# Optimization experiments

Measured on AMD Instinct MI355X. Metric: run time of the kernel, lower is better.

## Reference

```python
import jax, jax.numpy as jnp
import numpy as np

V = 32000   # vocab
D = 1024    # dim
H = 16      # query heads
HKV = 8     # kv heads (GQA)
DH = D // H # head dim = 64
L = 2       # layers
FF = 3584   # expert hidden dim
E = 8       # experts
K = 2       # top-k
EPS = 1e-5
BASE = 1000000.0
B, S = 1, 2048


def setup_inputs() -> dict:
    key = jax.random.key(0)
    ks = jax.random.split(key, 10)
    s = 0.02
    return {
        "x": jax.random.randint(ks[0], (B, S), 0, V, dtype=jnp.int64) if jax.config.jax_enable_x64 else jax.random.randint(ks[0], (B, S), 0, V),
        "emb": jax.random.normal(ks[1], (V, D), jnp.float32) * s,
        "ln_w": jnp.ones((L, D), jnp.float32),
        "ffln_w": jnp.ones((L, D), jnp.float32),
        "wq": jax.random.normal(ks[2], (L, D, H * DH), jnp.float32) * s,
        "wk": jax.random.normal(ks[3], (L, D, HKV * DH), jnp.float32) * s,
        "wv": jax.random.normal(ks[4], (L, D, HKV * DH), jnp.float32) * s,
        "wo": jax.random.normal(ks[5], (L, H * DH, D), jnp.float32) * s,
        "gate_w": jax.random.normal(ks[6], (L, E, D), jnp.float32) * s,
        "w1": jax.random.normal(ks[7], (L, E, FF, D), jnp.float32) * s,
        "w2": jax.random.normal(ks[8], (L, E, D, FF), jnp.float32) * s,
        "w3": jax.random.normal(ks[9], (L, E, FF, D), jnp.float32) * s,
        "dec_norm_w": jnp.ones((D,), jnp.float32),
    }


def rmsnorm(x, w):
    # LayerNormParameterized(use_mean=False, shift=False) == RMSNorm, pow in fp32
    xf = x.astype(jnp.float32)
    var = jnp.mean(xf * xf, axis=-1, keepdims=True)
    return ((xf * jax.lax.rsqrt(var + EPS)).astype(x.dtype)) * w


def rope(xh, pos):
    # interleaved (complex-pair) rotary embedding, xh: [B, S, h, DH]
    half = DH // 2
    freqs = 1.0 / (BASE ** (jnp.arange(0, half, dtype=jnp.float32) * 2.0 / DH))
    ang = pos[:, None] * freqs[None, :]                       # [S, half]
    cos = jnp.cos(ang)[None, :, None, :]
    sin = jnp.sin(ang)[None, :, None, :]
    x1 = xh[..., 0::2]
    x2 = xh[..., 1::2]
    out = jnp.stack([x1 * cos - x2 * sin, x1 * sin + x2 * cos], axis=-1)
    return out.reshape(xh.shape)


def reference(x, emb, ln_w, ffln_w, wq, wk, wv, wo, gate_w, w1, w2, w3, dec_norm_w):
    h = emb[x]                                                # [B, S, D]
    pos = jnp.arange(S, dtype=jnp.float32)
    causal = jnp.tril(jnp.ones((S, S), bool))[None, None]     # [1,1,S,S]
    scale = 1.0 / np.sqrt(DH).astype(np.float32)
    for i in range(L):
        # --- attention sub-layer ---
        res = h
        xn = rmsnorm(h, ln_w[i])
        q = rope((xn @ wq[i]).reshape(B, S, H, DH), pos)
        k = rope((xn @ wk[i]).reshape(B, S, HKV, DH), pos)
        v = (xn @ wv[i]).reshape(B, S, HKV, DH)
        rep = H // HKV
        k = jnp.repeat(k, rep, axis=2)                        # [B,S,H,DH]
        v = jnp.repeat(v, rep, axis=2)
        scores = jnp.einsum('bqhd,bkhd->bhqk', q, k) * scale
        scores = jnp.where(causal, scores, jnp.float32(-1e9))
        att = jax.nn.softmax(scores, axis=-1)
        o = jnp.einsum('bhqk,bkhd->bqhd', att, v).reshape(B, S, H * DH) @ wo[i]
        h = res + o
        # --- MoE FFN sub-layer ---
        res = h
        xn = rmsnorm(h, ffln_w[i]).reshape(B * S, D)          # [T, D]
        logits = xn @ gate_w[i].T                             # [T, E]
        gates = jax.nn.softmax(logits, axis=-1)
        topw, topi = jax.lax.top_k(gates, K)                  # [T, K]
        topw = topw / jnp.sum(topw, axis=-1, keepdims=True)
        # dense combine weights [T, E] (zero for unselected experts)
        cw = jnp.einsum('tk,tke->te', topw, jax.nn.one_hot(topi, E, dtype=topw.dtype))
        y = jnp.zeros_like(xn)
        for e in range(E):                                    # fixed small expert loop
            ye = (jax.nn.silu(xn @ w1[i, e].T) * (xn @ w3[i, e].T)) @ w2[i, e].T
            y = y + cw[:, e:e + 1] * ye
        h = res + y.reshape(B, S, D)
    return rmsnorm(h, dec_norm_w)
```

## Files before the change

### kernel.cpp

```cpp
#include <hip/hip_runtime.h>

using u16 = unsigned short;
using u32 = unsigned int;

#define TT 2048
#define DM 1024
#define NH 16
#define NKV 8
#define DHD 64
#define FFD 3584
#define NE 8

typedef __bf16 bf16x8 __attribute__((ext_vector_type(8)));
typedef float f32x4 __attribute__((ext_vector_type(4)));

__device__ __forceinline__ u16 f2bf(float x){
  return __builtin_bit_cast(u16, (__bf16)x);
}
__device__ __forceinline__ float bf2f(u16 h){
  return (float)__builtin_bit_cast(__bf16, h);
}
__device__ __forceinline__ f32x4 mfma16(bf16x8 a, bf16x8 b, f32x4 c){
  return __builtin_amdgcn_mfma_f32_16x16x32_bf16(a, b, c, 0, 0, 0);
}
__device__ __forceinline__ uint4 packhi8v(float4 a, float4 b){
  u16 h0=f2bf(a.x),h1=f2bf(a.y),h2=f2bf(a.z),h3=f2bf(a.w);
  u16 h4=f2bf(b.x),h5=f2bf(b.y),h6=f2bf(b.z),h7=f2bf(b.w);
  return make_uint4((u32)h0|((u32)h1<<16),(u32)h2|((u32)h3<<16),
                    (u32)h4|((u32)h5<<16),(u32)h6|((u32)h7<<16));
}
__device__ __forceinline__ uint4 packlo8v(float4 a, float4 b){
  u16 l0=f2bf(a.x-bf2f(f2bf(a.x))),l1=f2bf(a.y-bf2f(f2bf(a.y)));
  u16 l2=f2bf(a.z-bf2f(f2bf(a.z))),l3=f2bf(a.w-bf2f(f2bf(a.w)));
  u16 l4=f2bf(b.x-bf2f(f2bf(b.x))),l5=f2bf(b.y-bf2f(f2bf(b.y)));
  u16 l6=f2bf(b.z-bf2f(f2bf(b.z))),l7=f2bf(b.w-bf2f(f2bf(b.w)));
  return make_uint4((u32)l0|((u32)l1<<16),(u32)l2|((u32)l3<<16),
                    (u32)l4|((u32)l5<<16),(u32)l6|((u32)l7<<16));
}

#define SWZR(r) ((((r)>>1) ^ ((r)>>3)) & 3)
#define SWC(r,c) ((((c) ^ SWZR(r))) * 8)

__device__ __forceinline__ void glds16(const u16* g, u16* l){
  __builtin_amdgcn_global_load_lds(
      (const __attribute__((address_space(1))) void*)g,
      (__attribute__((address_space(3))) void*)l,
      16, 0, 0);
}

__global__ __launch_bounds__(256) void k_embed(const int* __restrict__ x,
    const float* __restrict__ emb, float* __restrict__ h){
  int t = blockIdx.x;
  int d = threadIdx.x * 4;
  float4 v = *reinterpret_cast<const float4*>(emb + (size_t)x[t] * DM + d);
  *reinterpret_cast<float4*>(h + (size_t)t * DM + d) = v;
}

template<int OUTF32>
__global__ __launch_bounds__(256) void k_rmsnorm(const float* __restrict__ in,
    const float* __restrict__ w, u16* __restrict__ oh, u16* __restrict__ ol,
    float* __restrict__ of){
  int t = blockIdx.x;
  int d4 = threadIdx.x * 4;
  float4 xv = *reinterpret_cast<const float4*>(in + (size_t)t * DM + d4);
  float ss = xv.x*xv.x + xv.y*xv.y + xv.z*xv.z + xv.w*xv.w;
#pragma unroll
  for (int m = 1; m < 64; m <<= 1) ss += __shfl_xor(ss, m);
  __shared__ float sred[4];
  if ((threadIdx.x & 63) == 0) sred[threadIdx.x >> 6] = ss;
  __syncthreads();
  float tot = sred[0] + sred[1] + sred[2] + sred[3];
  float r = 1.0f / sqrtf(tot * (1.0f / DM) + 1e-5f);
  float vv[4] = {xv.x, xv.y, xv.z, xv.w};
#pragma unroll
  for (int jj = 0; jj < 4; jj++){
    float xn = (vv[jj] * r) * w[d4 + jj];
    size_t a = (size_t)t * DM + d4 + jj;
    if constexpr (OUTF32){
      of[a] = xn;
    } else {
      u16 hi = f2bf(xn);
      oh[a] = hi;
      ol[a] = f2bf(xn - bf2f(hi));
    }
  }
}

__global__ __launch_bounds__(256) void k_trig(float* __restrict__ ct, float* __restrict__ st){
  int idx = blockIdx.x * 256 + threadIdx.x;
  int j = idx & 31;
  int s = idx >> 5;
  float xe = (float)j * 0.03125f;
  float yf = (float)pow(1.0e6, (double)xe);
  float fr = 1.0f / yf;
  float ang = (float)s * fr;
  double ad = (double)ang;
  ct[idx] = (float)cos(ad);
  st[idx] = (float)sin(ad);
}

template<int NHD>
__global__ __launch_bounds__(256) void k_rope(const float* __restrict__ in,
    const float* __restrict__ ct, const float* __restrict__ st,
    u16* __restrict__ oh, u16* __restrict__ ol){
  int idx = blockIdx.x * 256 + threadIdx.x;
  int j = idx & 31;
  int hd = (idx >> 5) % NHD;
  int s = idx / (32 * NHD);
  size_t base = ((size_t)s * NHD + hd) * 64 + 2 * j;
  float x1 = in[base], x2 = in[base + 1];
  int ti = (s << 5) | j;
  float c  = ct[ti];
  float sn = st[ti];
  float o1 = x1 * c - x2 * sn;
  float o2 = x1 * sn + x2 * c;
  u16 h1 = f2bf(o1), h2 = f2bf(o2);
  oh[base]     = h1; ol[base]     = f2bf(o1 - bf2f(h1));
  oh[base + 1] = h2; ol[base + 1] = f2bf(o2 - bf2f(h2));
}

__global__ __launch_bounds__(256) void k_splitbuf(const float* __restrict__ in,
    u16* __restrict__ oh, u16* __restrict__ ol, int n){
  int i = blockIdx.x * 256 + threadIdx.x;
  if (i < n){
    float x = in[i];
    u16 hi = f2bf(x);
    oh[i] = hi;
    ol[i] = f2bf(x - bf2f(hi));
  }
}

__global__ __launch_bounds__(256) void k_gate(const u16* __restrict__ xh,
    const u16* __restrict__ xl, const float* __restrict__ gw,
    int* __restrict__ topi, float* __restrict__ topw, int* __restrict__ cnt){
  int wv = threadIdx.x >> 6, lane = threadIdx.x & 63;
  int t = blockIdx.x * 4 + wv;
  float x[16];
#pragma unroll
  for (int i = 0; i < 16; i++){
    size_t a = (size_t)t * DM + lane + 64 * i;
    x[i] = bf2f(xh[a]) + bf2f(xl[a]);
  }
  float lgt[8];
#pragma unroll
  for (int e = 0; e < 8; e++){
    float s = 0.f;
#pragma unroll
    for (int i = 0; i < 16; i++) s += x[i] * gw[(size_t)e * DM + lane + 64 * i];
#pragma unroll
    for (int m = 1; m < 64; m <<= 1) s += __shfl_xor(s, m);
    lgt[e] = s;
  }
  float mx = lgt[0];
#pragma unroll
  for (int e = 1; e < 8; e++) mx = fmaxf(mx, lgt[e]);
  float p[8]; float sum = 0.f;
#pragma unroll
  for (int e = 0; e < 8; e++){ p[e] = expf(lgt[e] - mx); sum += p[e]; }
  float g[8];
#pragma unroll
  for (int e = 0; e < 8; e++) g[e] = p[e] / sum;
  int t0 = 0; float b0 = g[0];
#pragma unroll
  for (int e = 1; e < 8; e++) if (g[e] > b0){ b0 = g[e]; t0 = e; }
  int t1 = -1; float b1 = -1.f;
#pragma unroll
  for (int e = 0; e < 8; e++) if (e != t0 && g[e] > b1){ b1 = g[e]; t1 = e; }
  float ssum = b0 + b1;
  float w0 = b0 / ssum, w1 = b1 / ssum;
  if (lane == 0 && t < TT){
    topi[2*t] = t0; topi[2*t+1] = t1;
    topw[2*t] = w0; topw[2*t+1] = w1;
    atomicAdd(&cnt[t0], 1);
    atomicAdd(&cnt[t1], 1);
  }
}

__global__ void k_zero8(int* cnt){ if (threadIdx.x < 8) cnt[threadIdx.x] = 0; }

__global__ void k_scan(const int* __restrict__ cnt, int* __restrict__ offp, int* __restrict__ cur){
  if (threadIdx.x == 0){
    int r = 0;
    for (int e = 0; e < 8; e++){ offp[e] = r; r += cnt[e]; }
  }
  if (threadIdx.x < 8) cur[threadIdx.x] = 0;
}

__global__ __launch_bounds__(256) void k_scatter(const int* __restrict__ topi,
    const float* __restrict__ topw, const int* __restrict__ offp, int* __restrict__ cur,
    int* __restrict__ ftok, float* __restrict__ fwt){
  int t = blockIdx.x * 256 + threadIdx.x;
  if (t < TT){
#pragma unroll
    for (int j = 0; j < 2; j++){
      int e = topi[2*t + j];
      int p = atomicAdd(&cur[e], 1);
      ftok[offp[e] + p] = t;
      fwt[offp[e] + p] = topw[2*t + j];
    }
  }
}

#define GLDSA(BUF, KK) do { \
    glds16(Ah + gaA0 + (KK), (u16*)&Ash[BUF][awr0][0]); \
    glds16(Ah + gaA1 + (KK), (u16*)&Ash[BUF][awr1][0]); \
    if constexpr (SPLIT){ \
      glds16(Al + gaA0 + (KK), (u16*)&Asl[BUF][awr0][0]); \
      glds16(Al + gaA1 + (KK), (u16*)&Asl[BUF][awr1][0]); \
    } \
  } while(0)

#define GPRELOADB(KK) do { \
    if constexpr (BLAYOUT == 0){ \
      const float* bp_ = Bw + (size_t)(n0 + br0) * K + (KK) + cb8; \
      pB0 = *reinterpret_cast<const float4*>(bp_); \
      pB1 = *reinterpret_cast<const float4*>(bp_ + 4); \
      if constexpr (TN == 128){ \
        const float* bp2_ = Bw + (size_t)(n0 + br1) * K + (KK) + cb8; \
        pB2 = *reinterpret_cast<const float4*>(bp2_); \
        pB3 = *reinterpret_cast<const float4*>(bp2_ + 4); \
      } \
      if constexpr (DUAL){ \
        const float* bq_ = B3w + (size_t)(n0 + br0) * K + (KK) + cb8; \
        pB2 = *reinterpret_cast<const float4*>(bq_); \
        pB3 = *reinterpret_cast<const float4*>(bq_ + 4); \
      } \
    } else { \
      pB0 = *reinterpret_cast<const float4*>(Bw + (size_t)((KK) + kk1) * Nq + n0 + nn1); \
      pB1 = *reinterpret_cast<const float4*>(Bw + (size_t)((KK) + 16 + kk1) * Nq + n0 + nn1); \
    } \
  } while(0)

#define GSTOREB() do { \
    if constexpr (BLAYOUT == 0){ \
      *reinterpret_cast<uint4*>(&Bh1[br0][swB0]) = packhi8v(pB0, pB1); \
      if constexpr (SPLIT) *reinterpret_cast<uint4*>(&Bl1[br0][swB0]) = packlo8v(pB0, pB1); \
      if constexpr (TN == 128){ \
        *reinterpret_cast<uint4*>(&Bh1[br1][swB1]) = packhi8v(pB2, pB3); \
        if constexpr (SPLIT) *reinterpret_cast<uint4*>(&Bl1[br1][swB1]) = packlo8v(pB2, pB3); \
      } \
      if constexpr (DUAL){ \
        *reinterpret_cast<uint4*>(&Bh3[br0][swB0]) = packhi8v(pB2, pB3); \
        if constexpr (SPLIT) *reinterpret_cast<uint4*>(&Bl3[br0][swB0]) = packlo8v(pB2, pB3); \
      } \
    } else { \
      const float* q0 = reinterpret_cast<const float*>(&pB0); \
      const float* q1 = reinterpret_cast<const float*>(&pB1); \
      const int ch0 = kk1 >> 3, off0 = kk1 & 7; \
      _Pragma("unroll") \
      for (int j = 0; j < 4; j++){ \
        int row = nn1 + j; \
        int c0 = SWC(row, ch0) + off0; \
        int c1 = SWC(row, ch0 + 2) + off0; \
        u16 h0 = f2bf(q0[j]); \
        Bh1[row][c0] = h0; \
        if constexpr (SPLIT) Bl1[row][c0] = f2bf(q0[j] - bf2f(h0)); \
        u16 h1 = f2bf(q1[j]); \
        Bh1[row][c1] = h1; \
        if constexpr (SPLIT) Bl1[row][c1] = f2bf(q1[j] - bf2f(h1)); \
      } \
    } \
  } while(0)

#define MFMA_PHASE(CURB) do { \
    bf16x8 af[4], afl[4]; \
    _Pragma("unroll") \
    for (int m = 0; m < 4; m++){ \
      int Ra = wr*64 + m*16 + lr; \
      int sa = SWC(Ra, lg); \
      af[m] = *reinterpret_cast<const bf16x8*>(&Ash[CURB][Ra][sa]); \
      if constexpr (SPLIT) \
        afl[m] = *reinterpret_cast<const bf16x8*>(&Asl[CURB][Ra][sa]); \
    } \
    _Pragma("unroll") \
    for (int n = 0; n < NF; n++){ \
      int Rb = wc*(TN/2) + n*16 + lr; \
      int sb = SWC(Rb, lg); \
      bf16x8 b1 = *reinterpret_cast<const bf16x8*>(&Bh1[Rb][sb]); \
      _Pragma("unroll") \
      for (int m = 0; m < 4; m++) acc[m][n] = mfma16(af[m], b1, acc[m][n]); \
      if constexpr (SPLIT){ \
        bf16x8 bl = *reinterpret_cast<const bf16x8*>(&Bl1[Rb][sb]); \
        _Pragma("unroll") \
        for (int m = 0; m < 4; m++){ \
          acc[m][n] = mfma16(af[m], bl, acc[m][n]); \
          acc[m][n] = mfma16(afl[m], b1, acc[m][n]); \
        } \
      } \
      if constexpr (DUAL){ \
        bf16x8 b3 = *reinterpret_cast<const bf16x8*>(&Bh3[Rb][sb]); \
        _Pragma("unroll") \
        for (int m = 0; m < 4; m++) acc3[m][n] = mfma16(af[m], b3, acc3[m][n]); \
        if constexpr (SPLIT){ \
          bf16x8 b3l = *reinterpret_cast<const bf16x8*>(&Bl3[Rb][sb]); \
          _Pragma("unroll") \
          for (int m = 0; m < 4; m++){ \
            acc3[m][n] = mfma16(af[m], b3l, acc3[m][n]); \
            acc3[m][n] = mfma16(afl[m], b3, acc3[m][n]); \
          } \
        } \
      } \
    } \
  } while(0)

template<int BLAYOUT, int EPI, int SPLIT, int DUAL, int TN, int KS>
__global__ __launch_bounds__(256) void k_gemm(
    const u16* __restrict__ Ah, const u16* __restrict__ Al,
    const float* __restrict__ Bw, const float* __restrict__ B3w,
    const float* __restrict__ Bw2, const float* __restrict__ Bw3,
    size_t strideB, int N, int K,
    float* __restrict__ Cf, int ldc,
    float* __restrict__ Cf2, float* __restrict__ Cf3,
    u16* __restrict__ Ch, u16* __restrict__ Cl,
    const int* __restrict__ cntp, const int* __restrict__ offp,
    const int* __restrict__ ftok, const float* __restrict__ fwt)
{
  static_assert(!(DUAL && TN != 64), "DUAL uses TN=64");
  static_assert(!(BLAYOUT == 1 && TN != 64), "BLAYOUT=1 uses TN=64");
  int cnt = TT, off = 0, ks = 0;
  if constexpr (EPI == 2 || EPI == 3){
    int e = blockIdx.z / KS;
    ks = blockIdx.z % KS;
    cnt = cntp[e]; off = offp[e];
    if ((int)blockIdx.y * 128 >= cnt) return;
    Bw += (size_t)e * strideB;
    if constexpr (DUAL) B3w += (size_t)e * strideB;
  } else if constexpr (KS > 1){
    ks = blockIdx.z;
  }
  __shared__ u16 Ash[2][128][32];
  __shared__ u16 Asl[SPLIT ? 2 : 1][SPLIT ? 128 : 1][32];
  __shared__ u16 Bh1[TN][32];
  __shared__ u16 Bl1[SPLIT ? TN : 1][32];
  __shared__ u16 Bh3[DUAL ? TN : 1][32];
  __shared__ u16 Bl3[(DUAL && SPLIT) ? TN : 1][32];

  const int tid = threadIdx.x;
  const int m0 = blockIdx.y * 128;

  int n0, Nq = N, ldq = ldc;
  float* Cq = Cf;
  if constexpr (EPI == 4){
    int bx = blockIdx.x;
    if (bx < 16){       n0 = bx * 64;        Nq = 1024; ldq = 1024; Cq = Cf;  }
    else if (bx < 24){  n0 = (bx - 16) * 64; Nq = 512;  ldq = 512;  Cq = Cf2; Bw = Bw2; }
    else {              n0 = (bx - 24) * 64; Nq = 512;  ldq = 512;  Cq = Cf3; Bw = Bw3; }
  } else {
    n0 = blockIdx.x * TN;
  }

  const int wid = tid >> 6, lane = tid & 63;
  const int wr = wid >> 1, wc = wid & 1;
  const int lr = lane & 15, lg = lane >> 4;
  constexpr int NF = TN / 32;

  const int awr0 = wid * 32;
  const int awr1 = wid * 32 + 16;
  const int rA0 = awr0 + (lane >> 2);
  const int rA1 = awr1 + (lane >> 2);
  const int cA0 = (lane & 3) ^ SWZR(rA0);
  const int cA1 = (lane & 3) ^ SWZR(rA1);
  int grA0, grA1;
  {
    int g0 = m0 + rA0, g1 = m0 + rA1;
    if constexpr (EPI == 2){
      grA0 = ftok[off + (g0 < cnt ? g0 : cnt - 1)];
      grA1 = ftok[off + (g1 < cnt ? g1 : cnt - 1)];
    } else if constexpr (EPI == 3){
      grA0 = off + (g0 < cnt ? g0 : cnt - 1);
      grA1 = off + (g1 < cnt ? g1 : cnt - 1);
    } else {
      grA0 = g0; grA1 = g1;
    }
  }
  const size_t gaA0 = (size_t)grA0 * K + cA0 * 8;
  const size_t gaA1 = (size_t)grA1 * K + cA1 * 8;

  const int br0 = tid >> 2;
  const int br1 = br0 + 64;
  const int cb8 = (tid & 3) * 8;
  const int swB0 = SWC(br0, tid & 3), swB1 = SWC(br1, tid & 3);
  const int kk1 = tid >> 4;
  const int nn1 = (tid & 15) * 4;

  f32x4 acc[4][NF];
  f32x4 acc3[DUAL ? 4 : 1][NF];
#pragma unroll
  for (int m = 0; m < 4; m++)
#pragma unroll
    for (int n = 0; n < NF; n++){
      acc[m][n] = f32x4{0.f,0.f,0.f,0.f};
      if constexpr (DUAL) acc3[m][n] = f32x4{0.f,0.f,0.f,0.f};
    }

  float4 pB0{}, pB1{}, pB2{}, pB3{};

  const int kbeg = ks * (K / KS);
  const int kend = kbeg + (K / KS);

  GLDSA(0, kbeg);
  GPRELOADB(kbeg);
  int cur = 0;
  for (int k0 = kbeg; k0 < kend; k0 += 32){
    GSTOREB();
    asm volatile("s_waitcnt vmcnt(0) lgkmcnt(0)" ::: "memory");
    __builtin_amdgcn_s_barrier();
    if (k0 + 32 < kend){
      GLDSA(cur ^ 1, k0 + 32);
      GPRELOADB(k0 + 32);
    }
    MFMA_PHASE(cur);
    __builtin_amdgcn_s_barrier();
    cur ^= 1;
  }

#pragma unroll
  for (int m = 0; m < 4; m++)
#pragma unroll
    for (int n = 0; n < NF; n++)
#pragma unroll
      for (int r = 0; r < 4; r++){
        int row = m0 + wr*64 + m*16 + lg*4 + r;
        int col = n0 + wc*(TN/2) + n*16 + lr;
        float v = acc[m][n][r];
        if constexpr (EPI == 0){
          Cf[(size_t)row * ldc + col] = v;
        } else if constexpr (EPI == 1){
          if constexpr (KS > 1) atomicAdd(&Cf[(size_t)row * ldc + col], v);
          else                  Cf[(size_t)row * ldc + col] += v;
        } else if constexpr (EPI == 2){
          if (row < cnt){
            float a3 = acc3[m][n][r];
            float s = v / (1.0f + expf(-v));
            float y = s * a3;
            u16 hi = f2bf(y);
            size_t oa = (size_t)(off + row) * ldc + col;
            Ch[oa] = hi;
            Cl[oa] = f2bf(y - bf2f(hi));
          }
        } else if constexpr (EPI == 3){
          if (row < cnt){
            int tok = ftok[off + row];
            float wgt = fwt[off + row];
            atomicAdd(&Cf[(size_t)tok * ldc + col], wgt * v);
          }
        } else {
          if constexpr (KS > 1) atomicAdd(&Cq[(size_t)row * ldq + col], v);
          else                  Cq[(size_t)row * ldq + col] = v;
        }
      }
}

__global__ __launch_bounds__(256) void k_attn(
    const u16* __restrict__ qh, const u16* __restrict__ ql,
    const u16* __restrict__ kh, const u16* __restrict__ kl,
    const u16* __restrict__ vh, const u16* __restrict__ vl,
    u16* __restrict__ aoh, u16* __restrict__ aol)
{
  const int h  = blockIdx.y;
  const int q0 = blockIdx.x * 64;
  const int hk = h >> 1;
  const int tid = threadIdx.x;
  const int wv = tid >> 6, lane = tid & 63;
  const int lr = lane & 15, lg = lane >> 4;
  const int qw0 = q0 + wv * 16;

  __shared__ u16 Khs[32][72], Kls[32][72];
  __shared__ u16 Vhs[64][40], Vls[64][40];
  __shared__ u16 Phs[4][16][40], Pls[4][16][40];

  bf16x8 qfh[2], qfl[2];
#pragma unroll
  for (int dc = 0; dc < 2; dc++){
    size_t qa = ((size_t)(qw0 + lr) * NH + h) * 64 + dc*32 + lg*8;
    qfh[dc] = *reinterpret_cast<const bf16x8*>(qh + qa);
    qfl[dc] = *reinterpret_cast<const bf16x8*>(ql + qa);
  }
  f32x4 oacc[4];
  float mrun[4], lrun[4];
#pragma unroll
  for (int r = 0; r < 4; r++){ mrun[r] = -1e30f; lrun[r] = 0.f; }
#pragma unroll
  for (int g = 0; g < 4; g++) oacc[g] = f32x4{0.f,0.f,0.f,0.f};

  const int nt = q0 / 32 + 2;
  for (int kt = 0; kt < nt; kt++){
    int kg = kt * 32;
    {
      int kk = tid >> 3, c8 = (tid & 7) * 8;
      size_t ka = ((size_t)(kg + kk) * NKV + hk) * 64 + c8;
      *reinterpret_cast<uint4*>(&Khs[kk][c8]) = *reinterpret_cast<const uint4*>(kh + ka);
      *reinterpret_cast<uint4*>(&Kls[kk][c8]) = *reinterpret_cast<const uint4*>(kl + ka);
      uint4 v1 = *reinterpret_cast<const uint4*>(vh + ka);
      uint4 v2 = *reinterpret_cast<const uint4*>(vl + ka);
      const u16* p1 = reinterpret_cast<const u16*>(&v1);
      const u16* p2 = reinterpret_cast<const u16*>(&v2);
#pragma unroll
      for (int j = 0; j < 8; j++){ Vhs[c8 + j][kk] = p1[j]; Vls[c8 + j][kk] = p2[j]; }
    }
    __syncthreads();

    f32x4 sc[2];
    sc[0] = f32x4{0.f,0.f,0.f,0.f};
    sc[1] = f32x4{0.f,0.f,0.f,0.f};
#pragma unroll
    for (int c = 0; c < 2; c++){
#pragma unroll
      for (int dc = 0; dc < 2; dc++){
        bf16x8 bh = *reinterpret_cast<const bf16x8*>(&Khs[c*16 + lr][dc*32 + lg*8]);
        bf16x8 bl = *reinterpret_cast<const bf16x8*>(&Kls[c*16 + lr][dc*32 + lg*8]);
        sc[c] = mfma16(qfh[dc], bh, sc[c]);
        sc[c] = mfma16(qfh[dc], bl, sc[c]);
        sc[c] = mfma16(qfl[dc], bh, sc[c]);
      }
    }
    float pnew[2][4], corr[4];
#pragma unroll
    for (int r = 0; r < 4; r++){
      int row = qw0 + lg*4 + r;
      float s0 = (kg + lr      <= row) ? sc[0][r] * 0.125f : -1e30f;
      float s1 = (kg + 16 + lr <= row) ? sc[1][r] * 0.125f : -1e30f;
      float tm = fmaxf(s0, s1);
#pragma unroll
      for (int m = 1; m < 16; m <<= 1) tm = fmaxf(tm, __shfl_xor(tm, m));
      float mnew = fmaxf(mrun[r], tm);
      corr[r] = expf(mrun[r] - mnew);
      float p0 = expf(s0 - mnew);
      float p1 = expf(s1 - mnew);
      pnew[0][r] = p0; pnew[1][r] = p1;
      float sm = p0 + p1;
#pragma unroll
      for (int m = 1; m < 16; m <<= 1) sm += __shfl_xor(sm, m);
      lrun[r] = lrun[r] * corr[r] + sm;
      mrun[r] = mnew;
    }
#pragma unroll
    for (int g = 0; g < 4; g++){
      f32x4 t = oacc[g];
#pragma unroll
      for (int r = 0; r < 4; r++) t[r] *= corr[r];
      oacc[g] = t;
    }
#pragma unroll
    for (int c = 0; c < 2; c++)
#pragma unroll
      for (int r = 0; r < 4; r++){
        float p = pnew[c][r];
        u16 hi = f2bf(p);
        Phs[wv][lg*4 + r][c*16 + lr] = hi;
        Pls[wv][lg*4 + r][c*16 + lr] = f2bf(p - bf2f(hi));
      }
    asm volatile("s_waitcnt lgkmcnt(0)" ::: "memory");
    __builtin_amdgcn_sched_barrier(0);
    bf16x8 pah = *reinterpret_cast<const bf16x8*>(&Phs[wv][lr][lg*8]);
    bf16x8 pal = *reinterpret_cast<const bf16x8*>(&Pls[wv][lr][lg*8]);
#pragma unroll
    for (int g = 0; g < 4; g++){
      bf16x8 vb1 = *reinterpret_cast<const bf16x8*>(&Vhs[g*16 + lr][lg*8]);
      bf16x8 vb2 = *reinterpret_cast<const bf16x8*>(&Vls[g*16 + lr][lg*8]);
      oacc[g] = mfma16(pah, vb1, oacc[g]);
      oacc[g] = mfma16(pah, vb2, oacc[g]);
      oacc[g] = mfma16(pal, vb1, oacc[g]);
    }
    __syncthreads();
  }
#pragma unroll
  for (int g = 0; g < 4; g++)
#pragma unroll
    for (int r = 0; r < 4; r++){
      int row = qw0 + lg*4 + r;
      float v = oacc[g][r] / lrun[r];
      u16 hi = f2bf(v);
      size_t oa = ((size_t)row * NH + h) * 64 + g*16 + lr;
      aoh[oa] = hi;
      aol[oa] = f2bf(v - bf2f(hi));
    }
}

extern "C" void kernel_launch(void* const* d_in, const int* in_sizes, int n_in,
                              void* d_out, int out_size, void* d_ws, size_t ws_size,
                              hipStream_t stream){
  const int*   x     = (const int*)d_in[0];
  const float* emb   = (const float*)d_in[1];
  const float* lnw   = (const float*)d_in[2];
  const float* fflnw = (const float*)d_in[3];
  const float* wq    = (const float*)d_in[4];
  const float* wk    = (const float*)d_in[5];
  const float* wvp   = (const float*)d_in[6];
  const float* wo    = (const float*)d_in[7];
  const float* gw    = (const float*)d_in[8];
  const float* w1    = (const float*)d_in[9];
  const float* w2    = (const float*)d_in[10];
  const float* w3    = (const float*)d_in[11];
  const float* dnw   = (const float*)d_in[12];
  float* out = (float*)d_out;

  char* p = (char*)d_ws;
  auto alloc = [&](size_t bytes)->char*{
    char* r = p; p += (bytes + 255) & ~(size_t)255; return r;
  };
  float* h    = (float*)alloc((size_t)TT * DM * 4);
  float* qbuf = (float*)alloc((size_t)TT * 1024 * 4);
  float* kbuf = (float*)alloc((size_t)TT * 512 * 4);
  float* vbuf = (float*)alloc((size_t)TT * 512 * 4);
  u16* xnh = (u16*)alloc((size_t)TT * DM * 2);
  u16* xnl = (u16*)alloc((size_t)TT * DM * 2);
  u16* qhb = (u16*)alloc((size_t)TT * 1024 * 2);
  u16* qlb = (u16*)alloc((size_t)TT * 1024 * 2);
  u16* khb = (u16*)alloc((size_t)TT * 512 * 2);
  u16* klb = (u16*)alloc((size_t)TT * 512 * 2);
  u16* vhb = (u16*)alloc((size_t)TT * 512 * 2);
  u16* vlb = (u16*)alloc((size_t)TT * 512 * 2);
  u16* aoh = (u16*)alloc((size_t)TT * 1024 * 2);
  u16* aol = (u16*)alloc((size_t)TT * 1024 * 2);
  u16* acth = (u16*)alloc((size_t)2 * TT * FFD * 2);
  u16* actl = (u16*)alloc((size_t)2 * TT * FFD * 2);
  int*   topi = (int*)alloc((size_t)2 * TT * 4);
  float* topw = (float*)alloc((size_t)2 * TT * 4);
  int* cnt  = (int*)alloc(64);
  int* offe = (int*)alloc(64);
  int* cur  = (int*)alloc(64);
  int*   ftok = (int*)alloc((size_t)2 * TT * 4);
  float* fwt  = (float*)alloc((size_t)2 * TT * 4);
  float* ctab = (float*)aoh;
  float* stab = (float*)aol;

  k_embed<<<TT, 256, 0, stream>>>(x, emb, h);

  for (int i = 0; i < 2; i++){
    const float* wq_i = wq + (size_t)i * DM * 1024;
    const float* wk_i = wk + (size_t)i * DM * 512;
    const float* wv_i = wvp + (size_t)i * DM * 512;
    const float* wo_i = wo + (size_t)i * 1024 * DM;
    const float* w1_i = w1 + (size_t)i * NE * FFD * DM;
    const float* w2_i = w2 + (size_t)i * NE * DM * FFD;
    const float* w3_i = w3 + (size_t)i * NE * FFD * DM;

    k_rmsnorm<0><<<TT, 256, 0, stream>>>(h, lnw + i * DM, xnh, xnl, nullptr);

    hipMemsetAsync(qbuf, 0, (size_t)TT * 1024 * 4, stream);
    hipMemsetAsync(kbuf, 0, (size_t)TT * 512 * 4, stream);
    hipMemsetAsync(vbuf, 0, (size_t)TT * 512 * 4, stream);
    k_gemm<1,4,1,0,64,2><<<dim3(32,16,2), 256, 0, stream>>>(xnh, xnl,
        wq_i, nullptr, wk_i, wv_i, 0, 1024, DM,
        qbuf, 1024, kbuf, vbuf, nullptr, nullptr, nullptr, nullptr, nullptr, nullptr);

    k_trig<<<TT * 32 / 256, 256, 0, stream>>>(ctab, stab);
    k_rope<16><<<4096, 256, 0, stream>>>(qbuf, ctab, stab, qhb, qlb);
    k_rope<8><<<2048, 256, 0, stream>>>(kbuf, ctab, stab, khb, klb);
    k_splitbuf<<<4096, 256, 0, stream>>>(vbuf, vhb, vlb, TT * 512);

    k_attn<<<dim3(32,16,1), 256, 0, stream>>>(qhb, qlb, khb, klb, vhb, vlb, aoh, aol);

    k_gemm<1,1,1,0,64,2><<<dim3(16,16,2), 256, 0, stream>>>(aoh, aol,
        wo_i, nullptr, nullptr, nullptr, 0, DM, 1024,
        h, DM, nullptr, nullptr, nullptr, nullptr, nullptr, nullptr, nullptr, nullptr);

    k_rmsnorm<0><<<TT, 256, 0, stream>>>(h, fflnw + i * DM, xnh, xnl, nullptr);

    k_zero8<<<1, 64, 0, stream>>>(cnt);
    k_gate<<<TT/4, 256, 0, stream>>>(xnh, xnl, gw + (size_t)i * NE * DM, topi, topw, cnt);
    k_scan<<<1, 64, 0, stream>>>(cnt, offe, cur);
    k_scatter<<<8, 256, 0, stream>>>(topi, topw, offe, cur, ftok, fwt);

    if (i == 0){
      k_gemm<0,2,1,1,64,1><<<dim3(FFD/64,16,8), 256, 0, stream>>>(xnh, xnl,
          w1_i, w3_i, nullptr, nullptr, (size_t)FFD * DM, FFD, DM,
          nullptr, FFD, nullptr, nullptr, acth, actl, cnt, offe, ftok, fwt);
      k_gemm<0,3,1,0,128,4><<<dim3(DM/128,16,32), 256, 0, stream>>>(acth, actl,
          w2_i, nullptr, nullptr, nullptr, (size_t)DM * FFD, DM, FFD,
          h, DM, nullptr, nullptr, nullptr, nullptr, cnt, offe, ftok, fwt);
    } else {
      k_gemm<0,2,0,1,64,1><<<dim3(FFD/64,16,8), 256, 0, stream>>>(xnh, xnl,
          w1_i, w3_i, nullptr, nullptr, (size_t)FFD * DM, FFD, DM,
          nullptr, FFD, nullptr, nullptr, acth, actl, cnt, offe, ftok, fwt);
      k_gemm<0,3,0,0,128,4><<<dim3(DM/128,16,32), 256, 0, stream>>>(acth, actl,
          w2_i, nullptr, nullptr, nullptr, (size_t)DM * FFD, DM, FFD,
          h, DM, nullptr, nullptr, nullptr, nullptr, cnt, offe, ftok, fwt);
    }
  }

  k_rmsnorm<1><<<TT, 256, 0, stream>>>(h, dnw, nullptr, nullptr, out);
}
```

Measured before the change: 1.479 ms.

## Double-buffer B register prefetch to keep weight loads two K-steps ahead

The GEMM main loop now keeps two sets of B prefetch registers and unrolls by two K-steps. Global weight loads are issued two iterations ahead, and the wait uses a partial vmcnt so that the newest B loads can stay in flight across the barrier. The goal is to hide global-load latency on the fp32 weight stream. The cost is extra VGPRs for the second register set, which may lower occupancy. The correctness of the vmcnt counts depends on the order in which loads are issued.

Result: slower. 1.691 ms (+14.4%).

```diff
diff --git a/kernel.cpp b/kernel.cpp
--- a/kernel.cpp
+++ b/kernel.cpp
@@ -210,42 +210,42 @@
     } \
   } while(0)
 
-#define GPRELOADB(KK) do { \
+#define GPRELOADB(S, KK) do { \
     if constexpr (BLAYOUT == 0){ \
       const float* bp_ = Bw + (size_t)(n0 + br0) * K + (KK) + cb8; \
-      pB0 = *reinterpret_cast<const float4*>(bp_); \
-      pB1 = *reinterpret_cast<const float4*>(bp_ + 4); \
+      S##B0 = *reinterpret_cast<const float4*>(bp_); \
+      S##B1 = *reinterpret_cast<const float4*>(bp_ + 4); \
       if constexpr (TN == 128){ \
         const float* bp2_ = Bw + (size_t)(n0 + br1) * K + (KK) + cb8; \
-        pB2 = *reinterpret_cast<const float4*>(bp2_); \
-        pB3 = *reinterpret_cast<const float4*>(bp2_ + 4); \
+        S##B2 = *reinterpret_cast<const float4*>(bp2_); \
+        S##B3 = *reinterpret_cast<const float4*>(bp2_ + 4); \
       } \
       if constexpr (DUAL){ \
         const float* bq_ = B3w + (size_t)(n0 + br0) * K + (KK) + cb8; \
-        pB2 = *reinterpret_cast<const float4*>(bq_); \
-        pB3 = *reinterpret_cast<const float4*>(bq_ + 4); \
+        S##B2 = *reinterpret_cast<const float4*>(bq_); \
+        S##B3 = *reinterpret_cast<const float4*>(bq_ + 4); \
       } \
     } else { \
-      pB0 = *reinterpret_cast<const float4*>(Bw + (size_t)((KK) + kk1) * Nq + n0 + nn1); \
-      pB1 = *reinterpret_cast<const float4*>(Bw + (size_t)((KK) + 16 + kk1) * Nq + n0 + nn1); \
+      S##B0 = *reinterpret_cast<const float4*>(Bw + (size_t)((KK) + kk1) * Nq + n0 + nn1); \
+      S##B1 = *reinterpret_cast<const float4*>(Bw + (size_t)((KK) + 16 + kk1) * Nq + n0 + nn1); \
     } \
   } while(0)
 
-#define GSTOREB() do { \
+#define GSTOREB(S) do { \
     if constexpr (BLAYOUT == 0){ \
-      *reinterpret_cast<uint4*>(&Bh1[br0][swB0]) = packhi8v(pB0, pB1); \
-      if constexpr (SPLIT) *reinterpret_cast<uint4*>(&Bl1[br0][swB0]) = packlo8v(pB0, pB1); \
+      *reinterpret_cast<uint4*>(&Bh1[br0][swB0]) = packhi8v(S##B0, S##B1); \
+      if constexpr (SPLIT) *reinterpret_cast<uint4*>(&Bl1[br0][swB0]) = packlo8v(S##B0, S##B1); \
       if constexpr (TN == 128){ \
-        *reinterpret_cast<uint4*>(&Bh1[br1][swB1]) = packhi8v(pB2, pB3); \
-        if constexpr (SPLIT) *reinterpret_cast<uint4*>(&Bl1[br1][swB1]) = packlo8v(pB2, pB3); \
+        *reinterpret_cast<uint4*>(&Bh1[br1][swB1]) = packhi8v(S##B2, S##B3); \
+        if constexpr (SPLIT) *reinterpret_cast<uint4*>(&Bl1[br1][swB1]) = packlo8v(S##B2, S##B3); \
       } \
       if constexpr (DUAL){ \
-        *reinterpret_cast<uint4*>(&Bh3[br0][swB0]) = packhi8v(pB2, pB3); \
-        if constexpr (SPLIT) *reinterpret_cast<uint4*>(&Bl3[br0][swB0]) = packlo8v(pB2, pB3); \
+        *reinterpret_cast<uint4*>(&Bh3[br0][swB0]) = packhi8v(S##B2, S##B3); \
+        if constexpr (SPLIT) *reinterpret_cast<uint4*>(&Bl3[br0][swB0]) = packlo8v(S##B2, S##B3); \
       } \
     } else { \
-      const float* q0 = reinterpret_cast<const float*>(&pB0); \
-      const float* q1 = reinterpret_cast<const float*>(&pB1); \
+      const float* q0 = reinterpret_cast<const float*>(&S##B0); \
+      const float* q1 = reinterpret_cast<const float*>(&S##B1); \
       const int ch0 = kk1 >> 3, off0 = kk1 & 7; \
       _Pragma("unroll") \
       for (int j = 0; j < 4; j++){ \
@@ -261,6 +261,12 @@
       } \
     } \
   } while(0)
+
+#define WAITN() do { \
+    if constexpr (NBLD == 4) asm volatile("s_waitcnt vmcnt(4) lgkmcnt(0)" ::: "memory"); \
+    else                     asm volatile("s_waitcnt vmcnt(2) lgkmcnt(0)" ::: "memory"); \
+  } while(0)
+#define WAIT0() asm volatile("s_waitcnt vmcnt(0) lgkmcnt(0)" ::: "memory")
 
 #define MFMA_PHASE(CURB) do { \
     bf16x8 af[4], afl[4]; \
@@ -317,6 +323,7 @@
 {
   static_assert(!(DUAL && TN != 64), "DUAL uses TN=64");
   static_assert(!(BLAYOUT == 1 && TN != 64), "BLAYOUT=1 uses TN=64");
+  constexpr int NBLD = (BLAYOUT == 0 && (DUAL || TN == 128)) ? 4 : 2;
   int cnt = TT, off = 0, ks = 0;
   if constexpr (EPI == 2 || EPI == 3){
     int e = blockIdx.z / KS;
@@ -393,25 +400,39 @@
       if constexpr (DUAL) acc3[m][n] = f32x4{0.f,0.f,0.f,0.f};
     }
 
-  float4 pB0{}, pB1{}, pB2{}, pB3{};
+  float4 aB0{}, aB1{}, aB2{}, aB3{};
+  float4 bB0{}, bB1{}, bB2{}, bB3{};
 
   const int kbeg = ks * (K / KS);
   const int kend = kbeg + (K / KS);
 
   GLDSA(0, kbeg);
-  GPRELOADB(kbeg);
+  GPRELOADB(a, kbeg);
+  if (kbeg + 32 < kend) GPRELOADB(b, kbeg + 32);
   int cur = 0;
-  for (int k0 = kbeg; k0 < kend; k0 += 32){
-    GSTOREB();
-    asm volatile("s_waitcnt vmcnt(0) lgkmcnt(0)" ::: "memory");
-    __builtin_amdgcn_s_barrier();
+  for (int k0 = kbeg; k0 < kend; k0 += 64){
+    {
+      const bool pre = (k0 + 64 < kend);
+      GSTOREB(a);
+      if (pre) WAITN(); else WAIT0();
+      __builtin_amdgcn_s_barrier();
+      if (k0 + 32 < kend) GLDSA(cur ^ 1, k0 + 32);
+      if (pre) GPRELOADB(a, k0 + 64);
+      MFMA_PHASE(cur);
+      __builtin_amdgcn_s_barrier();
+      cur ^= 1;
+    }
     if (k0 + 32 < kend){
-      GLDSA(cur ^ 1, k0 + 32);
-      GPRELOADB(k0 + 32);
-    }
-    MFMA_PHASE(cur);
-    __builtin_amdgcn_s_barrier();
-    cur ^= 1;
+      const bool pre = (k0 + 96 < kend);
+      GSTOREB(b);
+      if (pre) WAITN(); else WAIT0();
+      __builtin_amdgcn_s_barrier();
+      if (k0 + 64 < kend) GLDSA(cur ^ 1, k0 + 64);
+      if (pre) GPRELOADB(b, k0 + 96);
+      MFMA_PHASE(cur);
+      __builtin_amdgcn_s_barrier();
+      cur ^= 1;
+    }
   }
 
 #pragma unroll
```
